# Optimization experiments

Hardware: AMD Instinct MI355X
Metric: run time of the kernel (lower is better)

## Reference

```python
import jax, jax.numpy as jnp
import numpy as np

D, NQ, BS, NL, NH, NP, DFF = 256, 900, 8, 4, 8, 4, 1024
HD = D // NH
SHAPES = np.array([[100, 100], [50, 50], [25, 25], [13, 13]], dtype=np.int64)  # (H, W) per level
LSTART = np.concatenate([[0], np.cumsum(SHAPES[:, 0] * SHAPES[:, 1])[:-1]]).astype(np.int64)
LMEM = int((SHAPES[:, 0] * SHAPES[:, 1]).sum())


def layer_norm(x, g, b, eps=1e-5):
    mu = x.mean(-1, keepdims=True)
    var = ((x - mu) ** 2).mean(-1, keepdims=True)
    return (x - mu) * jax.lax.rsqrt(var + eps) * g + b


def _forward(tgt, tgt_query_pos, tgt_reference_points, memory,
             in_proj_w, in_proj_b, out_proj_w, out_proj_b,
             samp_off_w, samp_off_b, attn_w_w, attn_w_b,
             value_proj_w, value_proj_b, output_proj_w, output_proj_b,
             lin1_w, lin1_b, lin2_w, lin2_b,
             norm1_g, norm1_b, norm2_g, norm2_b, norm3_g, norm3_b):
    # ---- self-attention (seq-first, torch nn.MultiheadAttention semantics) ----
    q = tgt + tgt_query_pos  # q = k = with_pos_embed(tgt, pos)
    Wq, Wk, Wv = jnp.split(in_proj_w, 3, 0)
    bq, bk, bv = jnp.split(in_proj_b, 3, 0)
    def heads(x):  # (nq, bs, d) -> (bs, nh, nq, hd)
        return x.reshape(NQ, BS, NH, HD).transpose(1, 2, 0, 3)
    qh = heads(q @ Wq.T + bq)
    kh = heads(q @ Wk.T + bk)
    vh = heads(tgt @ Wv.T + bv)
    attn = jax.nn.softmax(jnp.einsum('bhqd,bhkd->bhqk', qh, kh) / np.float32(np.sqrt(HD)), -1)
    sa = jnp.einsum('bhqk,bhkd->bhqd', attn, vh).transpose(2, 0, 1, 3).reshape(NQ, BS, D)
    sa = sa @ out_proj_w.T + out_proj_b
    t = layer_norm(tgt + sa, norm2_g, norm2_b)

    # ---- MSDeformAttn cross-attention (batch-first internally) ----
    qb = (t + tgt_query_pos).transpose(1, 0, 2)          # (bs, nq, d)
    refb = tgt_reference_points.transpose(1, 0, 2, 3)    # (bs, nq, nl, 2) in [0,1]
    memb = memory.transpose(1, 0, 2)                     # (bs, L, d)
    value = (memb @ value_proj_w.T + value_proj_b).reshape(BS, LMEM, NH, HD)
    off = (qb @ samp_off_w.T + samp_off_b).reshape(BS, NQ, NH, NL, NP, 2)
    aw = jax.nn.softmax((qb @ attn_w_w.T + attn_w_b).reshape(BS, NQ, NH, NL * NP), -1)
    aw = aw.reshape(BS, NQ, NH, NL, NP)
    normz = jnp.asarray(SHAPES[:, ::-1].copy(), dtype=jnp.float32)  # (nl, 2) = [W, H]
    loc = refb[:, :, None, :, None, :] + off / normz[None, None, None, :, None, :]

    out = jnp.zeros((BS, NQ, NH, HD), jnp.float32)
    for l in range(NL):  # fixed small number of pyramid levels
        Hl, Wl = int(SHAPES[l, 0]), int(SHAPES[l, 1])
        s = int(LSTART[l])
        v_l = value[:, s:s + Hl * Wl]  # (bs, Hl*Wl, nh, hd)
        # grid_sample(align_corners=False, padding=zeros) pixel coords
        x = (loc[:, :, :, l, :, 0] * Wl - 0.5).transpose(0, 1, 3, 2).reshape(BS, NQ * NP, NH)
        y = (loc[:, :, :, l, :, 1] * Hl - 0.5).transpose(0, 1, 3, 2).reshape(BS, NQ * NP, NH)
        x0 = jnp.floor(x)
        y0 = jnp.floor(y)
        samp = jnp.zeros((BS, NQ * NP, NH, HD), jnp.float32)
        for dx in (0, 1):
            for dy in (0, 1):
                xc = x0 + dx
                yc = y0 + dy
                w = (1.0 - jnp.abs(x - xc)) * (1.0 - jnp.abs(y - yc))
                valid = (xc >= 0) & (xc < Wl) & (yc >= 0) & (yc < Hl)
                idx = (jnp.clip(yc, 0, Hl - 1) * Wl + jnp.clip(xc, 0, Wl - 1)).astype(jnp.int32)
                g = jnp.take_along_axis(v_l, idx[..., None], axis=1)  # (bs, nq*np, nh, hd)
                samp = samp + jnp.where(valid, w, 0.0)[..., None] * g
        samp = samp.reshape(BS, NQ, NP, NH, HD)
        out = out + jnp.einsum('bqhp,bqphd->bqhd', aw[:, :, :, l], samp)
    ca = (out.reshape(BS, NQ, D) @ output_proj_w.T + output_proj_b).transpose(1, 0, 2)
    t = layer_norm(t + ca, norm1_g, norm1_b)

    # ---- FFN ----
    ffn = jax.nn.relu(t @ lin1_w.T + lin1_b) @ lin2_w.T + lin2_b
    return layer_norm(t + ffn, norm3_g, norm3_b)


def setup_inputs() -> dict:
    key = jax.random.key(0)
    ks = jax.random.split(key, 24)
    r = lambda i, shape, s: jax.random.normal(ks[i], shape, jnp.float32) * s
    return {
        'tgt': r(0, (NQ, BS, D), 1.0),
        'tgt_query_pos': r(1, (NQ, BS, D), 1.0),
        'tgt_reference_points': jax.random.uniform(ks[2], (NQ, BS, NL, 2), jnp.float32),
        'memory': r(3, (LMEM, BS, D), 1.0),
        'spatial_shapes': jnp.asarray(SHAPES),
        'level_start_index': jnp.asarray(LSTART),
        'in_proj_w': r(4, (3 * D, D), 0.02), 'in_proj_b': r(5, (3 * D,), 0.02),
        'out_proj_w': r(6, (D, D), 0.02), 'out_proj_b': r(7, (D,), 0.02),
        'samp_off_w': r(8, (NH * NL * NP * 2, D), 0.01), 'samp_off_b': r(9, (NH * NL * NP * 2,), 0.01),
        'attn_w_w': r(10, (NH * NL * NP, D), 0.02), 'attn_w_b': r(11, (NH * NL * NP,), 0.02),
        'value_proj_w': r(12, (D, D), 0.02), 'value_proj_b': r(13, (D,), 0.02),
        'output_proj_w': r(14, (D, D), 0.02), 'output_proj_b': r(15, (D,), 0.02),
        'lin1_w': r(16, (DFF, D), 0.02), 'lin1_b': r(17, (DFF,), 0.02),
        'lin2_w': r(18, (D, DFF), 0.02), 'lin2_b': r(19, (D,), 0.02),
        'norm1_g': jnp.ones((D,), jnp.float32), 'norm1_b': jnp.zeros((D,), jnp.float32),
        'norm2_g': jnp.ones((D,), jnp.float32), 'norm2_b': jnp.zeros((D,), jnp.float32),
        'norm3_g': jnp.ones((D,), jnp.float32), 'norm3_b': jnp.zeros((D,), jnp.float32),
    }


def reference(tgt, tgt_query_pos, tgt_reference_points, memory, spatial_shapes, level_start_index,
              in_proj_w, in_proj_b, out_proj_w, out_proj_b, samp_off_w, samp_off_b,
              attn_w_w, attn_w_b, value_proj_w, value_proj_b, output_proj_w, output_proj_b,
              lin1_w, lin1_b, lin2_w, lin2_b, norm1_g, norm1_b, norm2_g, norm2_b, norm3_g, norm3_b):
    # spatial_shapes / level_start_index are static level constants (module-level SHAPES/LSTART)
    return _forward(tgt, tgt_query_pos, tgt_reference_points, memory,
                    in_proj_w, in_proj_b, out_proj_w, out_proj_b,
                    samp_off_w, samp_off_b, attn_w_w, attn_w_b,
                    value_proj_w, value_proj_b, output_proj_w, output_proj_b,
                    lin1_w, lin1_b, lin2_w, lin2_b,
                    norm1_g, norm1_b, norm2_g, norm2_b, norm3_g, norm3_b)
```

## Files before the change

### kernel.cpp

```cpp
#include <hip/hip_runtime.h>
#include <hip/hip_bf16.h>


namespace {
constexpr int D_ = 256;
constexpr int NQ_ = 900;
constexpr int BS_ = 8;
constexpr int NH_ = 8;
constexpr int HD_ = 32;
constexpr int DFF_ = 1024;
constexpr int MTOK = NQ_ * BS_;
constexpr int LMEM_ = 13294;
constexpr long T = (long)MTOK * D_;
constexpr float QSC = 0.17677669529663687f;
constexpr int QKS = 512;
}

typedef __attribute__((ext_vector_type(8))) short bf8_t;
typedef __attribute__((ext_vector_type(4))) float f4_t;

#define MFMA16(a, b, c) __builtin_amdgcn_mfma_f32_16x16x32_bf16((a), (b), (c), 0, 0, 0)

__device__ __forceinline__ unsigned short bfbits(float x) {
    union { __hip_bfloat16 h; unsigned short u; } cv;
    cv.h = __float2bfloat16(x);
    return cv.u;
}
__device__ __forceinline__ float bf2f(unsigned short u) {
    union { float f; unsigned v; } cv;
    cv.v = ((unsigned)u) << 16;
    return cv.f;
}

__device__ __forceinline__ void gload16(const unsigned short* g, unsigned short* l) {
    __builtin_amdgcn_global_load_lds(
        (const __attribute__((address_space(1))) unsigned int*)(g),
        (__attribute__((address_space(3))) unsigned int*)(l), 16, 0, 0);
}

__global__ void conv_weights(
    const float* __restrict__ ipw, const float* __restrict__ opw,
    const float* __restrict__ sow, const float* __restrict__ aww,
    const float* __restrict__ vpw, const float* __restrict__ outpw,
    const float* __restrict__ l1w, const float* __restrict__ l2w,
    const float* __restrict__ ipb, const float* __restrict__ sob,
    const float* __restrict__ awb,
    unsigned short* __restrict__ Wbf, float* __restrict__ biasAll)
{
    if (blockIdx.x == 0) {
        for (int j = threadIdx.x; j < 512; j += 256)
            biasAll[j] = (j < 256) ? ipb[j] * QSC : ipb[j];
        for (int j = threadIdx.x; j < 384; j += 256)
            biasAll[512 + j] = (j < 256) ? sob[j] : awb[j - 256];
    }
    const long idx4 = (long)blockIdx.x * 256 + threadIdx.x;
    if (idx4 >= 253952) return;
    const long e = idx4 * 4;
    const float* src; long off; float sc = 1.f;
    if (e < 196608)      { src = ipw;   off = 0;      if (e < 65536) sc = QSC; }
    else if (e < 262144) { src = opw;   off = 196608; }
    else if (e < 327680) { src = sow;   off = 262144; }
    else if (e < 360448) { src = aww;   off = 327680; }
    else if (e < 425984) { src = vpw;   off = 360448; }
    else if (e < 491520) { src = outpw; off = 425984; }
    else if (e < 753664) { src = l1w;   off = 491520; }
    else                 { src = l2w;   off = 753664; }
    const float4 v = *(const float4*)(src + (e - off));
    union { unsigned short u[4]; uint2 w; } pk;
    pk.u[0] = bfbits(v.x * sc); pk.u[1] = bfbits(v.y * sc);
    pk.u[2] = bfbits(v.z * sc); pk.u[3] = bfbits(v.w * sc);
    *(uint2*)(Wbf + e) = pk.w;
}

template<bool RELU, bool OUTBF16>
__global__ __launch_bounds__(256) void gemm_mfma(
    const unsigned short* __restrict__ A, const unsigned short* __restrict__ W,
    const float* __restrict__ bias, void* __restrict__ C, int M, int N, int K)
{
    __shared__ unsigned short As[128 * 32];
    __shared__ unsigned short Ws[128 * 32];
    const int t = threadIdx.x;
    const long m0 = (long)blockIdx.x * 128;
    const int n0 = blockIdx.y * 128;
    const int row0 = t >> 2, cg = t & 3;
    long ar0 = m0 + row0;        if (ar0 > M - 1) ar0 = M - 1;
    long ar1 = m0 + 64 + row0;   if (ar1 > M - 1) ar1 = M - 1;
    const unsigned short* ga0 = A + ar0 * K + cg * 8;
    const unsigned short* ga1 = A + ar1 * K + cg * 8;
    const unsigned short* gw0 = W + (long)(n0 + row0) * K + cg * 8;
    const unsigned short* gw1 = W + (long)(n0 + 64 + row0) * K + cg * 8;
    unsigned short* la0 = As + t * 8;
    unsigned short* la1 = As + 2048 + t * 8;
    unsigned short* lw0 = Ws + t * 8;
    unsigned short* lw1 = Ws + 2048 + t * 8;
    const int lane = t & 63, wave = t >> 6;
    const int c = lane & 15, g = lane >> 4;
    const int wr = wave >> 1, wc = wave & 1;
    f4_t acc[4][4];
#pragma unroll
    for (int i = 0; i < 4; ++i)
#pragma unroll
        for (int j = 0; j < 4; ++j)
            acc[i][j] = f4_t{0.f, 0.f, 0.f, 0.f};

    for (int kb = 0; kb < K; kb += 32) {
        gload16(ga0 + kb, la0);
        gload16(ga1 + kb, la1);
        gload16(gw0 + kb, lw0);
        gload16(gw1 + kb, lw1);
        __syncthreads();
        bf8_t af[4], bfr[4];
#pragma unroll
        for (int i = 0; i < 4; ++i) {
            af[i] = *(const bf8_t*)(As + (wr * 64 + i * 16 + c) * 32 + g * 8);
            bfr[i] = *(const bf8_t*)(Ws + (wc * 64 + i * 16 + c) * 32 + g * 8);
        }
#pragma unroll
        for (int i = 0; i < 4; ++i)
#pragma unroll
            for (int j = 0; j < 4; ++j)
                acc[i][j] = MFMA16(af[i], bfr[j], acc[i][j]);
        __syncthreads();
    }

#pragma unroll
    for (int i = 0; i < 4; ++i) {
        const long rbase = m0 + wr * 64 + i * 16 + 4 * g;
#pragma unroll
        for (int j = 0; j < 4; ++j) {
            const int col = n0 + wc * 64 + j * 16 + c;
            const float bv = bias[col];
#pragma unroll
            for (int r = 0; r < 4; ++r) {
                const long rr = rbase + r;
                if (rr < M) {
                    float v = acc[i][j][r] + bv;
                    if (RELU) v = fmaxf(v, 0.f);
                    if (OUTBF16) ((unsigned short*)C)[rr * N + col] = bfbits(v);
                    else         ((float*)C)[rr * N + col] = v;
                }
            }
        }
    }
}

template<bool OUTBF16>
__global__ __launch_bounds__(256) void gemm_f32a(
    const float* __restrict__ A, const float* __restrict__ A2,
    const unsigned short* __restrict__ W, const float* __restrict__ bias,
    void* __restrict__ C, int M, int N, int K, int R1, int S1, int S2)
{
    __shared__ unsigned short As[128 * 32];
    __shared__ unsigned short Ws[128 * 32];
    const int t = threadIdx.x;
    const long m0 = (long)blockIdx.x * 128;
    const int n0 = blockIdx.y * 128;
    const int row0 = t >> 2, cg = t & 3;
    int gr0 = (int)m0 + row0;       if (gr0 > M - 1) gr0 = M - 1;
    int gr1 = (int)m0 + 64 + row0;  if (gr1 > M - 1) gr1 = M - 1;
    const long ar0 = (long)(gr0 / R1) * S1 + (long)(gr0 % R1) * S2;
    const long ar1 = (long)(gr1 / R1) * S1 + (long)(gr1 % R1) * S2;
    const float* Ap0 = A + ar0 * K + cg * 8;
    const float* Ap1 = A + ar1 * K + cg * 8;
    const float* Bp0 = A2 ? A2 + ar0 * K + cg * 8 : nullptr;
    const float* Bp1 = A2 ? A2 + ar1 * K + cg * 8 : nullptr;
    const unsigned short* gw0 = W + (long)(n0 + row0) * K + cg * 8;
    const unsigned short* gw1 = W + (long)(n0 + 64 + row0) * K + cg * 8;
    unsigned short* la0 = As + row0 * 32 + cg * 8;
    unsigned short* la1 = As + (64 + row0) * 32 + cg * 8;
    unsigned short* lw0 = Ws + t * 8;
    unsigned short* lw1 = Ws + 2048 + t * 8;
    const int lane = t & 63, wave = t >> 6;
    const int c = lane & 15, g = lane >> 4;
    const int wr = wave >> 1, wc = wave & 1;
    f4_t acc[4][4];
#pragma unroll
    for (int i = 0; i < 4; ++i)
#pragma unroll
        for (int j = 0; j < 4; ++j)
            acc[i][j] = f4_t{0.f, 0.f, 0.f, 0.f};

    for (int kb = 0; kb < K; kb += 32) {
        gload16(gw0 + kb, lw0);
        gload16(gw1 + kb, lw1);
        float4 a00 = *(const float4*)(Ap0 + kb);
        float4 a01 = *(const float4*)(Ap0 + kb + 4);
        float4 a10 = *(const float4*)(Ap1 + kb);
        float4 a11 = *(const float4*)(Ap1 + kb + 4);
        if (A2) {
            const float4 b00 = *(const float4*)(Bp0 + kb);
            const float4 b01 = *(const float4*)(Bp0 + kb + 4);
            const float4 b10 = *(const float4*)(Bp1 + kb);
            const float4 b11 = *(const float4*)(Bp1 + kb + 4);
            a00.x += b00.x; a00.y += b00.y; a00.z += b00.z; a00.w += b00.w;
            a01.x += b01.x; a01.y += b01.y; a01.z += b01.z; a01.w += b01.w;
            a10.x += b10.x; a10.y += b10.y; a10.z += b10.z; a10.w += b10.w;
            a11.x += b11.x; a11.y += b11.y; a11.z += b11.z; a11.w += b11.w;
        }
        union { bf8_t v; unsigned short u[8]; } p0, p1;
        p0.u[0] = bfbits(a00.x); p0.u[1] = bfbits(a00.y); p0.u[2] = bfbits(a00.z); p0.u[3] = bfbits(a00.w);
        p0.u[4] = bfbits(a01.x); p0.u[5] = bfbits(a01.y); p0.u[6] = bfbits(a01.z); p0.u[7] = bfbits(a01.w);
        p1.u[0] = bfbits(a10.x); p1.u[1] = bfbits(a10.y); p1.u[2] = bfbits(a10.z); p1.u[3] = bfbits(a10.w);
        p1.u[4] = bfbits(a11.x); p1.u[5] = bfbits(a11.y); p1.u[6] = bfbits(a11.z); p1.u[7] = bfbits(a11.w);
        *(bf8_t*)la0 = p0.v;
        *(bf8_t*)la1 = p1.v;
        __syncthreads();
        bf8_t af[4], bfr[4];
#pragma unroll
        for (int i = 0; i < 4; ++i) {
            af[i] = *(const bf8_t*)(As + (wr * 64 + i * 16 + c) * 32 + g * 8);
            bfr[i] = *(const bf8_t*)(Ws + (wc * 64 + i * 16 + c) * 32 + g * 8);
        }
#pragma unroll
        for (int i = 0; i < 4; ++i)
#pragma unroll
            for (int j = 0; j < 4; ++j)
                acc[i][j] = MFMA16(af[i], bfr[j], acc[i][j]);
        __syncthreads();
    }

#pragma unroll
    for (int i = 0; i < 4; ++i) {
        const long rbase = m0 + wr * 64 + i * 16 + 4 * g;
#pragma unroll
        for (int j = 0; j < 4; ++j) {
            const int col = n0 + wc * 64 + j * 16 + c;
            const float bv = bias[col];
#pragma unroll
            for (int r = 0; r < 4; ++r) {
                const long rr = rbase + r;
                if (rr < M) {
                    float v = acc[i][j][r] + bv;
                    if (OUTBF16) ((unsigned short*)C)[rr * N + col] = bfbits(v);
                    else         ((float*)C)[rr * N + col] = v;
                }
            }
        }
    }
}

__global__ __launch_bounds__(256) void attn_mfma(
    const unsigned short* __restrict__ Qb, const unsigned short* __restrict__ Kb,
    const unsigned short* __restrict__ Vb, unsigned short* __restrict__ sa)
{
    __shared__ float smemf[2112];
    unsigned short* Ks = (unsigned short*)smemf;
    unsigned short* Vt = (unsigned short*)(smemf + 1024);
    const int t = threadIdx.x;
    const int wave = t >> 6, lane = t & 63;
    const int g = lane >> 4, c = lane & 15;
    const int b = blockIdx.x >> 3, h = blockIdx.x & 7;
    const int q0 = blockIdx.y * 64 + wave * 16;
    const int q = q0 + c;
    const bool qv = q < NQ_;
    const bf8_t qf = *(const bf8_t*)(Qb + ((long)(qv ? q : 0) * BS_ + b) * QKS + h * HD_ + 8 * g);

    f4_t acc0 = {0.f, 0.f, 0.f, 0.f}, acc1 = {0.f, 0.f, 0.f, 0.f};
    float m_run = -1e30f, l_run = 0.f;
    const int sk = t >> 2, sd = (t & 3) * 8;

    for (int kc = 0; kc < NQ_; kc += 64) {
        __syncthreads();
        {
            const int key = kc + sk;
            union { bf8_t v; unsigned short u[8]; } kv, vv;
            if (key < NQ_) {
                kv.v = *(const bf8_t*)(Kb + ((long)key * BS_ + b) * QKS + h * HD_ + sd);
                vv.v = *(const bf8_t*)(Vb + ((long)key * BS_ + b) * D_ + h * HD_ + sd);
            } else {
#pragma unroll
                for (int u = 0; u < 8; ++u) { kv.u[u] = 0; vv.u[u] = 0; }
            }
            *(bf8_t*)(Ks + sk * 32 + sd) = kv.v;
#pragma unroll
            for (int u = 0; u < 8; ++u) {
                const int r = sd + u;
                Vt[r * 64 + (sk ^ ((r & 7) << 3))] = vv.u[u];
            }
        }
        __syncthreads();

        f4_t s[4];
#pragma unroll
        for (int tt = 0; tt < 4; ++tt) {
            const bf8_t kf = *(const bf8_t*)(Ks + (tt * 16 + c) * 32 + 8 * g);
            f4_t z = {0.f, 0.f, 0.f, 0.f};
            s[tt] = MFMA16(kf, qf, z);
        }
        float sv[16];
#pragma unroll
        for (int tt = 0; tt < 4; ++tt)
#pragma unroll
            for (int r = 0; r < 4; ++r) {
                float x = s[tt][r];
                if (kc + tt * 16 + 4 * g + r >= NQ_) x = -1e30f;
                sv[tt * 4 + r] = x;
            }
        float mloc = sv[0];
#pragma unroll
        for (int i = 1; i < 16; ++i) mloc = fmaxf(mloc, sv[i]);
        mloc = fmaxf(mloc, __shfl_xor(mloc, 16));
        mloc = fmaxf(mloc, __shfl_xor(mloc, 32));
        const float mnew = fmaxf(m_run, mloc);
        const float resc = __expf(m_run - mnew);
        float p[16], ls = 0.f;
#pragma unroll
        for (int i = 0; i < 16; ++i) { p[i] = __expf(sv[i] - mnew); ls += p[i]; }
        ls += __shfl_xor(ls, 16);
        ls += __shfl_xor(ls, 32);
        l_run = l_run * resc + ls;
        m_run = mnew;
#pragma unroll
        for (int r = 0; r < 4; ++r) { acc0[r] *= resc; acc1[r] *= resc; }

        unsigned pk[4][2];
#pragma unroll
        for (int tt = 0; tt < 4; ++tt) {
            pk[tt][0] = (unsigned)bfbits(p[tt * 4 + 0]) | ((unsigned)bfbits(p[tt * 4 + 1]) << 16);
            pk[tt][1] = (unsigned)bfbits(p[tt * 4 + 2]) | ((unsigned)bfbits(p[tt * 4 + 3]) << 16);
        }
        const int srcA = ((g & 1) << 5) + c;
        const int srcB = srcA + 16;
#pragma unroll
        for (int kh = 0; kh < 2; ++kh) {
            const unsigned a0 = __shfl(pk[kh * 2][0], srcA), b0_ = __shfl(pk[kh * 2 + 1][0], srcA);
            const unsigned a1 = __shfl(pk[kh * 2][1], srcA), b1_ = __shfl(pk[kh * 2 + 1][1], srcA);
            const unsigned a2 = __shfl(pk[kh * 2][0], srcB), b2_ = __shfl(pk[kh * 2 + 1][0], srcB);
            const unsigned a3 = __shfl(pk[kh * 2][1], srcB), b3_ = __shfl(pk[kh * 2 + 1][1], srcB);
            union { bf8_t v; unsigned u[4]; } pf;
            const bool hi = (g & 2);
            pf.u[0] = hi ? b0_ : a0; pf.u[1] = hi ? b1_ : a1;
            pf.u[2] = hi ? b2_ : a2; pf.u[3] = hi ? b3_ : a3;
            const int kcol = (kh * 32 + 8 * g) ^ ((c & 7) << 3);
            const bf8_t vf0 = *(const bf8_t*)(Vt + c * 64 + kcol);
            const bf8_t vf1 = *(const bf8_t*)(Vt + (16 + c) * 64 + kcol);
            acc0 = MFMA16(vf0, pf.v, acc0);
            acc1 = MFMA16(vf1, pf.v, acc1);
        }
    }

    __syncthreads();
    const float invl = 1.f / l_run;
    float* O = smemf + wave * 528;
#pragma unroll
    for (int r = 0; r < 4; ++r) {
        O[c * 33 + 4 * g + r] = acc0[r] * invl;
        O[c * 33 + 16 + 4 * g + r] = acc1[r] * invl;
    }
    __syncthreads();
    {
        const int ql = lane >> 2, part = lane & 3;
        const int qg = q0 + ql;
        if (qg < NQ_) {
            union { bf8_t v; unsigned short u[8]; } pk;
#pragma unroll
            for (int u = 0; u < 8; ++u) pk.u[u] = bfbits(O[ql * 33 + part * 8 + u]);
            *(bf8_t*)(sa + ((long)qg * BS_ + b) * D_ + h * HD_ + part * 8) = pk.v;
        }
    }
}

__global__ __launch_bounds__(256) void msdeform_kernel(
    const float* __restrict__ oa, const float* __restrict__ refp,
    const unsigned short* __restrict__ val, unsigned short* __restrict__ out)
{
    __shared__ float saw[128];
    __shared__ float redm[8], redi[8];
    __shared__ float swt[128][4];
    __shared__ int sidx[128][4];
    const int bq = blockIdx.x;
    const int b = bq / NQ_, q = bq % NQ_;
    const int t = threadIdx.x;
    if (t < 128) saw[t] = oa[(long)bq * 384 + 256 + t];
    __syncthreads();
    if (t < 8) {
        float mx = -1e30f;
        for (int i = 0; i < 16; ++i) mx = fmaxf(mx, saw[t * 16 + i]);
        float s = 0.f;
        for (int i = 0; i < 16; ++i) s += __expf(saw[t * 16 + i] - mx);
        redm[t] = mx; redi[t] = 1.f / s;
    }
    __syncthreads();
    if (t < 128) {
        const int h = t >> 4, lp = t & 15, l = lp >> 2, p = lp & 3;
        const float aw = __expf(saw[t] - redm[h]) * redi[h];
        const int Wi = (l == 0) ? 100 : (l == 1) ? 50 : (l == 2) ? 25 : 13;
        const int Hi = Wi;
        const int sl = (l == 0) ? 0 : (l == 1) ? 10000 : (l == 2) ? 12500 : 13125;
        const float offx = oa[(long)bq * 384 + h * 32 + l * 8 + p * 2 + 0];
        const float offy = oa[(long)bq * 384 + h * 32 + l * 8 + p * 2 + 1];
        const float refx = refp[(((long)q * BS_ + b) * 4 + l) * 2 + 0];
        const float refy = refp[(((long)q * BS_ + b) * 4 + l) * 2 + 1];
        const float fW = (float)Wi, fH = (float)Hi;
        const float x = (refx + offx / fW) * fW - 0.5f;
        const float y = (refy + offy / fH) * fH - 0.5f;
        const float x0f = floorf(x), y0f = floorf(y);
        const float fx = x - x0f, fy = y - y0f;
        const int ix = (int)x0f, iy = (int)y0f;
        const float wts[4] = {(1.f - fx) * (1.f - fy), fx * (1.f - fy),
                              (1.f - fx) * fy,          fx * fy};
        const int xs[4] = {ix, ix + 1, ix, ix + 1};
        const int ys[4] = {iy, iy, iy + 1, iy + 1};
#pragma unroll
        for (int tap = 0; tap < 4; ++tap) {
            const bool valid = (xs[tap] >= 0) & (xs[tap] < Wi) & (ys[tap] >= 0) & (ys[tap] < Hi);
            const int xc = min(max(xs[tap], 0), Wi - 1);
            const int yc = min(max(ys[tap], 0), Hi - 1);
            swt[t][tap] = valid ? aw * wts[tap] : 0.f;
            sidx[t][tap] = b * LMEM_ + sl + yc * Wi + xc;
        }
    }
    __syncthreads();
    const int h = t >> 5, r = t & 31, qd = r & 7, s = r >> 3;
    float a0 = 0.f, a1 = 0.f, a2 = 0.f, a3 = 0.f;
#pragma unroll
    for (int i = 0; i < 16; ++i) {
        const int j = h * 16 + i;
        const float wv = swt[j][s];
        const long base = (long)sidx[j][s] * D_ + h * HD_ + qd * 4;
        const uint2 raw = *(const uint2*)(val + base);
        a0 += wv * bf2f((unsigned short)(raw.x & 0xffff));
        a1 += wv * bf2f((unsigned short)(raw.x >> 16));
        a2 += wv * bf2f((unsigned short)(raw.y & 0xffff));
        a3 += wv * bf2f((unsigned short)(raw.y >> 16));
    }
    a0 += __shfl_xor(a0, 8); a0 += __shfl_xor(a0, 16);
    a1 += __shfl_xor(a1, 8); a1 += __shfl_xor(a1, 16);
    a2 += __shfl_xor(a2, 8); a2 += __shfl_xor(a2, 16);
    a3 += __shfl_xor(a3, 8); a3 += __shfl_xor(a3, 16);
    if (s == 0) {
        union { unsigned short u[4]; uint2 w; } pk;
        pk.u[0] = bfbits(a0); pk.u[1] = bfbits(a1); pk.u[2] = bfbits(a2); pk.u[3] = bfbits(a3);
        *(uint2*)(out + (long)bq * D_ + h * HD_ + qd * 4) = pk.w;
    }
}

__global__ __launch_bounds__(256) void ln_kernel(
    const float* __restrict__ inA, const float* __restrict__ inB,
    const float* __restrict__ g, const float* __restrict__ be,
    float* __restrict__ out, const float* __restrict__ pos,
    unsigned short* __restrict__ bfOut, int swapB, int bfMode)
{
    const int r = blockIdx.x * 4 + (threadIdx.x >> 6);
    const int lane = threadIdx.x & 63;
    long rb = r;
    if (swapB) rb = (long)(r & 7) * NQ_ + (r >> 3);
    const float4 a4 = *(const float4*)(inA + (long)r * D_ + lane * 4);
    const float4 b4 = *(const float4*)(inB + rb * D_ + lane * 4);
    float x[4] = {a4.x + b4.x, a4.y + b4.y, a4.z + b4.z, a4.w + b4.w};
    float s = x[0] + x[1] + x[2] + x[3];
#pragma unroll
    for (int off = 32; off > 0; off >>= 1) s += __shfl_xor(s, off);
    const float mu = s * (1.f / D_);
    float v = 0.f;
#pragma unroll
    for (int cc = 0; cc < 4; ++cc) { const float dd = x[cc] - mu; v += dd * dd; }
#pragma unroll
    for (int off = 32; off > 0; off >>= 1) v += __shfl_xor(v, off);
    const float rs = rsqrtf(v * (1.f / D_) + 1e-5f);
    const float4 g4 = *(const float4*)(g + lane * 4);
    const float4 e4 = *(const float4*)(be + lane * 4);
    const float gg[4] = {g4.x, g4.y, g4.z, g4.w};
    const float ee[4] = {e4.x, e4.y, e4.z, e4.w};
    float y[4];
#pragma unroll
    for (int cc = 0; cc < 4; ++cc) y[cc] = (x[cc] - mu) * rs * gg[cc] + ee[cc];
    *(float4*)(out + (long)r * D_ + lane * 4) = make_float4(y[0], y[1], y[2], y[3]);
    if (bfMode) {
        float z[4] = {y[0], y[1], y[2], y[3]};
        long er = r;
        if (bfMode == 2) {
            const float4 p4 = *(const float4*)(pos + (long)r * D_ + lane * 4);
            z[0] += p4.x; z[1] += p4.y; z[2] += p4.z; z[3] += p4.w;
            er = (long)(r & 7) * NQ_ + (r >> 3);
        }
        union { unsigned short u[4]; uint2 w; } pk;
        pk.u[0] = bfbits(z[0]); pk.u[1] = bfbits(z[1]);
        pk.u[2] = bfbits(z[2]); pk.u[3] = bfbits(z[3]);
        *(uint2*)(bfOut + er * D_ + lane * 4) = pk.w;
    }
}

extern "C" void kernel_launch(void* const* d_in, const int* in_sizes, int n_in,
                              void* d_out, int out_size, void* d_ws, size_t ws_size,
                              hipStream_t stream) {
    const float* tgt   = (const float*)d_in[0];
    const float* pos   = (const float*)d_in[1];
    const float* refp  = (const float*)d_in[2];
    const float* mem   = (const float*)d_in[3];
    const float* ipw   = (const float*)d_in[6];
    const float* ipb   = (const float*)d_in[7];
    const float* opw   = (const float*)d_in[8];
    const float* opb   = (const float*)d_in[9];
    const float* sow   = (const float*)d_in[10];
    const float* sob   = (const float*)d_in[11];
    const float* aww   = (const float*)d_in[12];
    const float* awb   = (const float*)d_in[13];
    const float* vpw   = (const float*)d_in[14];
    const float* vpb   = (const float*)d_in[15];
    const float* outpw = (const float*)d_in[16];
    const float* outpb = (const float*)d_in[17];
    const float* l1w   = (const float*)d_in[18];
    const float* l1b   = (const float*)d_in[19];
    const float* l2w   = (const float*)d_in[20];
    const float* l2b   = (const float*)d_in[21];
    const float* n1g = (const float*)d_in[22]; const float* n1be = (const float*)d_in[23];
    const float* n2g = (const float*)d_in[24]; const float* n2be = (const float*)d_in[25];
    const float* n3g = (const float*)d_in[26]; const float* n3be = (const float*)d_in[27];

    char* wsb = (char*)d_ws;
    auto alloc = [&](size_t bytes) { char* p = wsb; wsb += (bytes + 255) & ~(size_t)255; return p; };
    unsigned short* Wbf       = (unsigned short*)alloc(1015808 * 2);
    float*          biasAll   = (float*)alloc(896 * 4);
    unsigned short* QK_bf     = (unsigned short*)alloc(T * 4);
    unsigned short* Vb_bf     = (unsigned short*)alloc(T * 2);
    unsigned short* sa_bf     = (unsigned short*)alloc(T * 2);
    float*          saproj    = (float*)alloc(T * 4);
    float*          t1        = (float*)alloc(T * 4);
    unsigned short* qplus2_bf = (unsigned short*)alloc(T * 2);
    float*          oa        = (float*)alloc((long)MTOK * 384 * 4);
    unsigned short* sampo_bf  = (unsigned short*)alloc(T * 2);
    float*          ca        = (float*)alloc(T * 4);
    float*          t2        = (float*)alloc(T * 4);
    unsigned short* t2_bf     = (unsigned short*)alloc(T * 2);
    unsigned short* ffnh_bf   = (unsigned short*)alloc((long)MTOK * DFF_ * 2);
    float*          ffno      = (float*)alloc(T * 4);
    unsigned short* val       = (unsigned short*)alloc((long)BS_ * LMEM_ * D_ * 2);
    const unsigned short* wqk   = Wbf + 0;
    const unsigned short* wv    = Wbf + 131072;
    const unsigned short* wo    = Wbf + 196608;
    const unsigned short* wsoaw = Wbf + 262144;
    const unsigned short* wvp   = Wbf + 360448;
    const unsigned short* wop   = Wbf + 425984;
    const unsigned short* wl1   = Wbf + 491520;
    const unsigned short* wl2   = Wbf + 753664;
    const float* bias_qk = biasAll;
    const float* bias_oa = biasAll + 512;

    const dim3 blk(256);
    const dim3 g_m(57, 2);

    conv_weights<<<992, blk, 0, stream>>>(ipw, opw, sow, aww, vpw, outpw, l1w, l2w,
                                          ipb, sob, awb, Wbf, biasAll);
    gemm_f32a<true><<<dim3(57, 4), blk, 0, stream>>>(tgt, pos, wqk, bias_qk, QK_bf,
                                                     MTOK, QKS, D_, MTOK, 0, 1);
    gemm_f32a<true><<<g_m, blk, 0, stream>>>(tgt, nullptr, wv, ipb + 2 * D_, Vb_bf,
                                             MTOK, D_, D_, MTOK, 0, 1);
    attn_mfma<<<dim3(64, 15), blk, 0, stream>>>(QK_bf, QK_bf + 256, Vb_bf, sa_bf);
    gemm_mfma<false, false><<<g_m, blk, 0, stream>>>(sa_bf, wo, opb, saproj, MTOK, D_, D_);
    ln_kernel<<<1800, blk, 0, stream>>>(tgt, saproj, n2g, n2be, t1, pos, qplus2_bf, 0, 2);
    gemm_f32a<true><<<dim3(831, 2), blk, 0, stream>>>(mem, nullptr, wvp, vpb, val,
                                                      BS_ * LMEM_, D_, D_, LMEM_, 1, BS_);
    gemm_mfma<false, false><<<dim3(57, 3), blk, 0, stream>>>(qplus2_bf, wsoaw, bias_oa, oa, MTOK, 384, D_);
    msdeform_kernel<<<7200, blk, 0, stream>>>(oa, refp, val, sampo_bf);
    gemm_mfma<false, false><<<g_m, blk, 0, stream>>>(sampo_bf, wop, outpb, ca, MTOK, D_, D_);
    ln_kernel<<<1800, blk, 0, stream>>>(t1, ca, n1g, n1be, t2, nullptr, t2_bf, 1, 1);
    gemm_mfma<true, true><<<dim3(57, 8), blk, 0, stream>>>(t2_bf, wl1, l1b, ffnh_bf, MTOK, DFF_, D_);
    gemm_mfma<false, false><<<g_m, blk, 0, stream>>>(ffnh_bf, wl2, l2b, ffno, MTOK, D_, DFF_);
    ln_kernel<<<1800, blk, 0, stream>>>(t2, ffno, n3g, n3be, (float*)d_out, nullptr, nullptr, 0, 0);
}
```

Measured before the change: 258.5 us.

## Swizzle GEMM LDS layouts and load fp32 A tiles directly to LDS

Applies an XOR swizzle to the LDS tile layouts in all GEMM kernels, so the MFMA fragment reads avoid bank conflicts. The global source addresses are permuted so the linear direct-to-LDS stores land in swizzled order. Adds a gemm_f32d kernel that streams fp32 activations straight into LDS with global_load_lds and converts them to bf16 at fragment-read time. This removes the register round-trip for the V projection and the large memory value projection. The trade-off is double the LDS footprint for the A tile and bf16 conversion repeated on every fragment read.

```diff
diff --git a/kernel.cpp b/kernel.cpp
--- a/kernel.cpp
+++ b/kernel.cpp
@@ -33,6 +33,11 @@
 }
 
 __device__ __forceinline__ void gload16(const unsigned short* g, unsigned short* l) {
+    __builtin_amdgcn_global_load_lds(
+        (const __attribute__((address_space(1))) unsigned int*)(g),
+        (__attribute__((address_space(3))) unsigned int*)(l), 16, 0, 0);
+}
+__device__ __forceinline__ void gload16f(const float* g, float* l) {
     __builtin_amdgcn_global_load_lds(
         (const __attribute__((address_space(1))) unsigned int*)(g),
         (__attribute__((address_space(3))) unsigned int*)(l), 16, 0, 0);
@@ -82,20 +87,18 @@
     const int t = threadIdx.x;
     const long m0 = (long)blockIdx.x * 128;
     const int n0 = blockIdx.y * 128;
-    const int row0 = t >> 2, cg = t & 3;
+    const int row0 = t >> 2;
+    const int cgp = (t & 3) ^ ((t >> 2) & 3);
     long ar0 = m0 + row0;        if (ar0 > M - 1) ar0 = M - 1;
     long ar1 = m0 + 64 + row0;   if (ar1 > M - 1) ar1 = M - 1;
-    const unsigned short* ga0 = A + ar0 * K + cg * 8;
-    const unsigned short* ga1 = A + ar1 * K + cg * 8;
-    const unsigned short* gw0 = W + (long)(n0 + row0) * K + cg * 8;
-    const unsigned short* gw1 = W + (long)(n0 + 64 + row0) * K + cg * 8;
-    unsigned short* la0 = As + t * 8;
-    unsigned short* la1 = As + 2048 + t * 8;
-    unsigned short* lw0 = Ws + t * 8;
-    unsigned short* lw1 = Ws + 2048 + t * 8;
+    const unsigned short* ga0 = A + ar0 * K + cgp * 8;
+    const unsigned short* ga1 = A + ar1 * K + cgp * 8;
+    const unsigned short* gw0 = W + (long)(n0 + row0) * K + cgp * 8;
+    const unsigned short* gw1 = W + (long)(n0 + 64 + row0) * K + cgp * 8;
     const int lane = t & 63, wave = t >> 6;
     const int c = lane & 15, g = lane >> 4;
     const int wr = wave >> 1, wc = wave & 1;
+    const int sws = (g * 8) ^ ((c & 3) * 8);
     f4_t acc[4][4];
 #pragma unroll
     for (int i = 0; i < 4; ++i)
@@ -104,16 +107,16 @@
             acc[i][j] = f4_t{0.f, 0.f, 0.f, 0.f};
 
     for (int kb = 0; kb < K; kb += 32) {
-        gload16(ga0 + kb, la0);
-        gload16(ga1 + kb, la1);
-        gload16(gw0 + kb, lw0);
-        gload16(gw1 + kb, lw1);
+        gload16(ga0 + kb, As + t * 8);
+        gload16(ga1 + kb, As + 2048 + t * 8);
+        gload16(gw0 + kb, Ws + t * 8);
+        gload16(gw1 + kb, Ws + 2048 + t * 8);
         __syncthreads();
         bf8_t af[4], bfr[4];
 #pragma unroll
         for (int i = 0; i < 4; ++i) {
-            af[i] = *(const bf8_t*)(As + (wr * 64 + i * 16 + c) * 32 + g * 8);
-            bfr[i] = *(const bf8_t*)(Ws + (wc * 64 + i * 16 + c) * 32 + g * 8);
+            af[i] = *(const bf8_t*)(As + (wr * 64 + i * 16 + c) * 32 + sws);
+            bfr[i] = *(const bf8_t*)(Ws + (wc * 64 + i * 16 + c) * 32 + sws);
         }
 #pragma unroll
         for (int i = 0; i < 4; ++i)
@@ -145,10 +148,100 @@
 }
 
 template<bool OUTBF16>
+__global__ __launch_bounds__(256) void gemm_f32d(
+    const float* __restrict__ A, const unsigned short* __restrict__ W,
+    const float* __restrict__ bias, void* __restrict__ C,
+    int M, int N, int K, int R1, int S1, int S2)
+{
+    __shared__ float Asf[128 * 32];
+    __shared__ unsigned short Ws[128 * 32];
+    const int t = threadIdx.x;
+    const long m0 = (long)blockIdx.x * 128;
+    const int n0 = blockIdx.y * 128;
+    const int spA = (t & 7) ^ ((t >> 3) & 7);
+    const float *gA0, *gA1, *gA2, *gA3;
+    {
+        int r0 = (int)m0 + 0  + (t >> 3); if (r0 > M - 1) r0 = M - 1;
+        int r1 = (int)m0 + 32 + (t >> 3); if (r1 > M - 1) r1 = M - 1;
+        int r2 = (int)m0 + 64 + (t >> 3); if (r2 > M - 1) r2 = M - 1;
+        int r3 = (int)m0 + 96 + (t >> 3); if (r3 > M - 1) r3 = M - 1;
+        gA0 = A + ((long)(r0 / R1) * S1 + (long)(r0 % R1) * S2) * K + spA * 4;
+        gA1 = A + ((long)(r1 / R1) * S1 + (long)(r1 % R1) * S2) * K + spA * 4;
+        gA2 = A + ((long)(r2 / R1) * S1 + (long)(r2 % R1) * S2) * K + spA * 4;
+        gA3 = A + ((long)(r3 / R1) * S1 + (long)(r3 % R1) * S2) * K + spA * 4;
+    }
+    const int row0 = t >> 2;
+    const int cgp = (t & 3) ^ ((t >> 2) & 3);
+    const unsigned short* gw0 = W + (long)(n0 + row0) * K + cgp * 8;
+    const unsigned short* gw1 = W + (long)(n0 + 64 + row0) * K + cgp * 8;
+    const int lane = t & 63, wave = t >> 6;
+    const int c = lane & 15, g = lane >> 4;
+    const int wr = wave >> 1, wc = wave & 1;
+    const int s0 = (2 * g) ^ (c & 7);
+    const int s1 = (2 * g + 1) ^ (c & 7);
+    const int sws = (g * 8) ^ ((c & 3) * 8);
+    f4_t acc[4][4];
+#pragma unroll
+    for (int i = 0; i < 4; ++i)
+#pragma unroll
+        for (int j = 0; j < 4; ++j)
+            acc[i][j] = f4_t{0.f, 0.f, 0.f, 0.f};
+
+    for (int kb = 0; kb < K; kb += 32) {
+        gload16f(gA0 + kb, Asf + t * 4);
+        gload16f(gA1 + kb, Asf + 1024 + t * 4);
+        gload16f(gA2 + kb, Asf + 2048 + t * 4);
+        gload16f(gA3 + kb, Asf + 3072 + t * 4);
+        gload16(gw0 + kb, Ws + t * 8);
+        gload16(gw1 + kb, Ws + 2048 + t * 8);
+        __syncthreads();
+        bf8_t af[4], bfr[4];
+#pragma unroll
+        for (int i = 0; i < 4; ++i) {
+            const int row = wr * 64 + i * 16 + c;
+            const f4_t lo = *(const f4_t*)(Asf + row * 32 + s0 * 4);
+            const f4_t hi = *(const f4_t*)(Asf + row * 32 + s1 * 4);
+            union { bf8_t v; unsigned short u[8]; } pk;
+            pk.u[0] = bfbits(lo[0]); pk.u[1] = bfbits(lo[1]);
+            pk.u[2] = bfbits(lo[2]); pk.u[3] = bfbits(lo[3]);
+            pk.u[4] = bfbits(hi[0]); pk.u[5] = bfbits(hi[1]);
+            pk.u[6] = bfbits(hi[2]); pk.u[7] = bfbits(hi[3]);
+            af[i] = pk.v;
+            bfr[i] = *(const bf8_t*)(Ws + (wc * 64 + i * 16 + c) * 32 + sws);
+        }
+#pragma unroll
+        for (int i = 0; i < 4; ++i)
+#pragma unroll
+            for (int j = 0; j < 4; ++j)
+                acc[i][j] = MFMA16(af[i], bfr[j], acc[i][j]);
+        __syncthreads();
+    }
+
+#pragma unroll
+    for (int i = 0; i < 4; ++i) {
+        const long rbase = m0 + wr * 64 + i * 16 + 4 * g;
+#pragma unroll
+        for (int j = 0; j < 4; ++j) {
+            const int col = n0 + wc * 64 + j * 16 + c;
+            const float bv = bias[col];
+#pragma unroll
+            for (int r = 0; r < 4; ++r) {
+                const long rr = rbase + r;
+                if (rr < M) {
+                    float v = acc[i][j][r] + bv;
+                    if (OUTBF16) ((unsigned short*)C)[rr * N + col] = bfbits(v);
+                    else         ((float*)C)[rr * N + col] = v;
+                }
+            }
+        }
+    }
+}
+
+template<bool OUTBF16>
 __global__ __launch_bounds__(256) void gemm_f32a(
     const float* __restrict__ A, const float* __restrict__ A2,
     const unsigned short* __restrict__ W, const float* __restrict__ bias,
-    void* __restrict__ C, int M, int N, int K, int R1, int S1, int S2)
+    void* __restrict__ C, int M, int N, int K)
 {
     __shared__ unsigned short As[128 * 32];
     __shared__ unsigned short Ws[128 * 32];
@@ -156,23 +249,21 @@
     const long m0 = (long)blockIdx.x * 128;
     const int n0 = blockIdx.y * 128;
     const int row0 = t >> 2, cg = t & 3;
-    int gr0 = (int)m0 + row0;       if (gr0 > M - 1) gr0 = M - 1;
-    int gr1 = (int)m0 + 64 + row0;  if (gr1 > M - 1) gr1 = M - 1;
-    const long ar0 = (long)(gr0 / R1) * S1 + (long)(gr0 % R1) * S2;
-    const long ar1 = (long)(gr1 / R1) * S1 + (long)(gr1 % R1) * S2;
+    const int cgp = cg ^ ((t >> 2) & 3);
+    long ar0 = m0 + row0;        if (ar0 > M - 1) ar0 = M - 1;
+    long ar1 = m0 + 64 + row0;   if (ar1 > M - 1) ar1 = M - 1;
     const float* Ap0 = A + ar0 * K + cg * 8;
     const float* Ap1 = A + ar1 * K + cg * 8;
-    const float* Bp0 = A2 ? A2 + ar0 * K + cg * 8 : nullptr;
-    const float* Bp1 = A2 ? A2 + ar1 * K + cg * 8 : nullptr;
-    const unsigned short* gw0 = W + (long)(n0 + row0) * K + cg * 8;
-    const unsigned short* gw1 = W + (long)(n0 + 64 + row0) * K + cg * 8;
-    unsigned short* la0 = As + row0 * 32 + cg * 8;
-    unsigned short* la1 = As + (64 + row0) * 32 + cg * 8;
-    unsigned short* lw0 = Ws + t * 8;
-    unsigned short* lw1 = Ws + 2048 + t * 8;
+    const float* Bp0 = A2 + ar0 * K + cg * 8;
+    const float* Bp1 = A2 + ar1 * K + cg * 8;
+    const unsigned short* gw0 = W + (long)(n0 + row0) * K + cgp * 8;
+    const unsigned short* gw1 = W + (long)(n0 + 64 + row0) * K + cgp * 8;
+    unsigned short* la0 = As + row0 * 32 + ((cg * 8) ^ ((row0 & 3) * 8));
+    unsigned short* la1 = la0 + 2048;
     const int lane = t & 63, wave = t >> 6;
     const int c = lane & 15, g = lane >> 4;
     const int wr = wave >> 1, wc = wave & 1;
+    const int sws = (g * 8) ^ ((c & 3) * 8);
     f4_t acc[4][4];
 #pragma unroll
     for (int i = 0; i < 4; ++i)
@@ -181,35 +272,33 @@
             acc[i][j] = f4_t{0.f, 0.f, 0.f, 0.f};
 
     for (int kb = 0; kb < K; kb += 32) {
-        gload16(gw0 + kb, lw0);
-        gload16(gw1 + kb, lw1);
-        float4 a00 = *(const float4*)(Ap0 + kb);
-        float4 a01 = *(const float4*)(Ap0 + kb + 4);
-        float4 a10 = *(const float4*)(Ap1 + kb);
-        float4 a11 = *(const float4*)(Ap1 + kb + 4);
-        if (A2) {
-            const float4 b00 = *(const float4*)(Bp0 + kb);
-            const float4 b01 = *(const float4*)(Bp0 + kb + 4);
-            const float4 b10 = *(const float4*)(Bp1 + kb);
-            const float4 b11 = *(const float4*)(Bp1 + kb + 4);
-            a00.x += b00.x; a00.y += b00.y; a00.z += b00.z; a00.w += b00.w;
-            a01.x += b01.x; a01.y += b01.y; a01.z += b01.z; a01.w += b01.w;
-            a10.x += b10.x; a10.y += b10.y; a10.z += b10.z; a10.w += b10.w;
-            a11.x += b11.x; a11.y += b11.y; a11.z += b11.z; a11.w += b11.w;
-        }
+        gload16(gw0 + kb, Ws + t * 8);
+        gload16(gw1 + kb, Ws + 2048 + t * 8);
+        const float4 a00 = *(const float4*)(Ap0 + kb);
+        const float4 a01 = *(const float4*)(Ap0 + kb + 4);
+        const float4 a10 = *(const float4*)(Ap1 + kb);
+        const float4 a11 = *(const float4*)(Ap1 + kb + 4);
+        const float4 b00 = *(const float4*)(Bp0 + kb);
+        const float4 b01 = *(const float4*)(Bp0 + kb + 4);
+        const float4 b10 = *(const float4*)(Bp1 + kb);
+        const float4 b11 = *(const float4*)(Bp1 + kb + 4);
         union { bf8_t v; unsigned short u[8]; } p0, p1;
-        p0.u[0] = bfbits(a00.x); p0.u[1] = bfbits(a00.y); p0.u[2] = bfbits(a00.z); p0.u[3] = bfbits(a00.w);
-        p0.u[4] = bfbits(a01.x); p0.u[5] = bfbits(a01.y); p0.u[6] = bfbits(a01.z); p0.u[7] = bfbits(a01.w);
-        p1.u[0] = bfbits(a10.x); p1.u[1] = bfbits(a10.y); p1.u[2] = bfbits(a10.z); p1.u[3] = bfbits(a10.w);
-        p1.u[4] = bfbits(a11.x); p1.u[5] = bfbits(a11.y); p1.u[6] = bfbits(a11.z); p1.u[7] = bfbits(a11.w);
+        p0.u[0] = bfbits(a00.x + b00.x); p0.u[1] = bfbits(a00.y + b00.y);
+        p0.u[2] = bfbits(a00.z + b00.z); p0.u[3] = bfbits(a00.w + b00.w);
+        p0.u[4] = bfbits(a01.x + b01.x); p0.u[5] = bfbits(a01.y + b01.y);
+        p0.u[6] = bfbits(a01.z + b01.z); p0.u[7] = bfbits(a01.w + b01.w);
+        p1.u[0] = bfbits(a10.x + b10.x); p1.u[1] = bfbits(a10.y + b10.y);
+        p1.u[2] = bfbits(a10.z + b10.z); p1.u[3] = bfbits(a10.w + b10.w);
+        p1.u[4] = bfbits(a11.x + b11.x); p1.u[5] = bfbits(a11.y + b11.y);
+        p1.u[6] = bfbits(a11.z + b11.z); p1.u[7] = bfbits(a11.w + b11.w);
         *(bf8_t*)la0 = p0.v;
         *(bf8_t*)la1 = p1.v;
         __syncthreads();
         bf8_t af[4], bfr[4];
 #pragma unroll
         for (int i = 0; i < 4; ++i) {
-            af[i] = *(const bf8_t*)(As + (wr * 64 + i * 16 + c) * 32 + g * 8);
-            bfr[i] = *(const bf8_t*)(Ws + (wc * 64 + i * 16 + c) * 32 + g * 8);
+            af[i] = *(const bf8_t*)(As + (wr * 64 + i * 16 + c) * 32 + sws);
+            bfr[i] = *(const bf8_t*)(Ws + (wc * 64 + i * 16 + c) * 32 + sws);
         }
 #pragma unroll
         for (int i = 0; i < 4; ++i)
@@ -543,13 +632,13 @@
     conv_weights<<<992, blk, 0, stream>>>(ipw, opw, sow, aww, vpw, outpw, l1w, l2w,
                                           ipb, sob, awb, Wbf, biasAll);
     gemm_f32a<true><<<dim3(57, 4), blk, 0, stream>>>(tgt, pos, wqk, bias_qk, QK_bf,
-                                                     MTOK, QKS, D_, MTOK, 0, 1);
-    gemm_f32a<true><<<g_m, blk, 0, stream>>>(tgt, nullptr, wv, ipb + 2 * D_, Vb_bf,
+                                                     MTOK, QKS, D_);
+    gemm_f32d<true><<<g_m, blk, 0, stream>>>(tgt, wv, ipb + 2 * D_, Vb_bf,
                                              MTOK, D_, D_, MTOK, 0, 1);
     attn_mfma<<<dim3(64, 15), blk, 0, stream>>>(QK_bf, QK_bf + 256, Vb_bf, sa_bf);
     gemm_mfma<false, false><<<g_m, blk, 0, stream>>>(sa_bf, wo, opb, saproj, MTOK, D_, D_);
     ln_kernel<<<1800, blk, 0, stream>>>(tgt, saproj, n2g, n2be, t1, pos, qplus2_bf, 0, 2);
-    gemm_f32a<true><<<dim3(831, 2), blk, 0, stream>>>(mem, nullptr, wvp, vpb, val,
+    gemm_f32d<true><<<dim3(831, 2), blk, 0, stream>>>(mem, wvp, vpb, val,
                                                       BS_ * LMEM_, D_, D_, LMEM_, 1, BS_);
     gemm_mfma<false, false><<<dim3(57, 3), blk, 0, stream>>>(qplus2_bf, wsoaw, bias_oa, oa, MTOK, 384, D_);
     msdeform_kernel<<<7200, blk, 0, stream>>>(oa, refp, val, sampo_bf);
```

Result: no change. 261.0 us (+1.0%).
